# Optimization experiments

Hardware: AMD Instinct MI355X
Metric: run time of the kernel (lower is better)

The kernel has to match this reference:

```python
import jax, jax.numpy as jnp
import numpy as np

N_NODES = 50000
N_EDGES = 800000
IN_CH = 128
HID = 64
PROJ = 32


def _gcn_norm(edge_index, n):
    # add self loops, symmetric normalization D^-1/2 (A+I) D^-1/2
    loop = jnp.arange(n, dtype=edge_index.dtype)
    src = jnp.concatenate([edge_index[0], loop])
    dst = jnp.concatenate([edge_index[1], loop])
    deg = jax.ops.segment_sum(jnp.ones_like(dst, jnp.float32), dst, num_segments=n)
    dinv = deg ** -0.5  # deg >= 1 due to self loops
    norm = dinv[src] * dinv[dst]
    return src, dst, norm


def _propagate(h, src, dst, norm, n):
    # gather -> scale -> scatter-add (message passing along A_hat)
    return jax.ops.segment_sum(h[src] * norm[:, None], dst, num_segments=n)


def _ho_gcn_layer(x, src, dst, norm, Ws, b, n):
    # out = sum_{k=1..max_order} (A_hat^k x) W_k + b
    out = jnp.zeros((n, Ws[0].shape[1]), x.dtype)
    h = x
    for W in Ws:
        h = _propagate(h, src, dst, norm, n)
        out = out + h @ W
    return out + b


def setup_inputs() -> dict:
    key = jax.random.key(0)
    ks = jax.random.split(key, 16)

    def w(k, fan_in, fan_out):
        return (jax.random.normal(k, (fan_in, fan_out), jnp.float32) / np.sqrt(fan_in)).astype(jnp.float32)

    x = jax.random.normal(ks[0], (N_NODES, IN_CH), jnp.float32)
    edge_index = jax.random.randint(ks[1], (2, N_EDGES), 0, N_NODES, dtype=jnp.int64)
    return {
        "x": x,
        "edge_index": edge_index,
        # conv1: max_order=2 -> two weights
        "W1_1": w(ks[2], IN_CH, HID), "W1_2": w(ks[3], IN_CH, HID),
        "b1": jnp.zeros((HID,), jnp.float32),
        # conv2
        "W2_1": w(ks[4], HID, HID // 2), "W2_2": w(ks[5], HID, HID // 2),
        "b2": jnp.zeros((HID // 2,), jnp.float32),
        # projection head
        "Wp1": w(ks[6], HID // 2, PROJ), "bp1": jnp.zeros((PROJ,), jnp.float32),
        "Wp2": w(ks[7], PROJ, PROJ), "bp2": jnp.zeros((PROJ,), jnp.float32),
        # coordinate head
        "Wc1": w(ks[8], HID // 2, HID // 4), "bc1": jnp.zeros((HID // 4,), jnp.float32),
        "Wc2": w(ks[9], HID // 4, 2), "bc2": jnp.zeros((2,), jnp.float32),
    }


def reference(x, edge_index, W1_1, W1_2, b1, W2_1, W2_2, b2,
              Wp1, bp1, Wp2, bp2, Wc1, bc1, Wc2, bc2):
    n = x.shape[0]
    src, dst, norm = _gcn_norm(edge_index, n)
    h1 = jax.nn.relu(_ho_gcn_layer(x, src, dst, norm, (W1_1, W1_2), b1, n))
    # dropout is identity in eval/reference mode
    h2 = jax.nn.relu(_ho_gcn_layer(h1, src, dst, norm, (W2_1, W2_2), b2, n))
    z = jax.nn.relu(h2 @ Wp1 + bp1) @ Wp2 + bp2
    coordinates = jax.nn.relu(h2 @ Wc1 + bc1) @ Wc2 + bc2
    return (coordinates, z)
```

## Files before the change

### kernel.cpp

```cpp
#include <hip/hip_runtime.h>
#include <hip/hip_fp16.h>

#define NN 50000
#define NE 800000
#define S 4
#define BINW 12500
#define NN4 (NN * S)
#define NBLK2 ((NN4 + 255) / 256)
#define NBG ((NN + 63) / 64)
#define NBH4 ((NE / 4 + 255) / 256)
#define COLCAP (NE + 3 * NN4 + 8)

__device__ __forceinline__ float4 ldh4(const __half2* p) {
    float2 raw = *(const float2*)p;
    __half2 a = *(__half2*)&raw.x;
    __half2 b = *(__half2*)&raw.y;
    float2 fa = __half22float2(a);
    float2 fb = __half22float2(b);
    return make_float4(fa.x, fa.y, fb.x, fb.y);
}
__device__ __forceinline__ void sth4(__half2* p, float4 v) {
    __half2 a = __floats2half2_rn(v.x, v.y);
    __half2 b = __floats2half2_rn(v.z, v.w);
    float2 raw;
    raw.x = *(float*)&a; raw.y = *(float*)&b;
    *(float2*)p = raw;
}

__global__ __launch_bounds__(256) void hist_k(const int* __restrict__ src,
                                              const int* __restrict__ dst,
                                              int* __restrict__ cnt,
                                              int* __restrict__ rank) {
    int e = (blockIdx.x * 256 + threadIdx.x) * 4;
    if (e >= NE) return;
    int4 s4 = *(const int4*)(src + e);
    int4 d4 = *(const int4*)(dst + e);
    int4 r;
    r.x = atomicAdd(&cnt[d4.x * S + s4.x / BINW], 1);
    r.y = atomicAdd(&cnt[d4.y * S + s4.y / BINW], 1);
    r.z = atomicAdd(&cnt[d4.z * S + s4.z / BINW], 1);
    r.w = atomicAdd(&cnt[d4.w * S + s4.w / BINW], 1);
    *(int4*)(rank + e) = r;
}

__global__ __launch_bounds__(256) void sum_blocks_k(const int* __restrict__ cnt,
                                                    int* __restrict__ bsum,
                                                    float* __restrict__ dinv,
                                                    unsigned* __restrict__ y2h_s,
                                                    unsigned* __restrict__ uh_s,
                                                    unsigned* __restrict__ z2h_s,
                                                    unsigned* __restrict__ u2h_s) {
    __shared__ int s[256];
    int t = threadIdx.x;
    int i = blockIdx.x * 256 + t;
    if (blockIdx.x == 0) {
        if (t < 32) { y2h_s[t] = 0u; uh_s[t] = 0u; }
        else if (t < 48) { z2h_s[t - 32] = 0u; u2h_s[t - 32] = 0u; }
    }
    int v = 0;
    if (i < NN4) {
        int c = cnt[i];
        v = (c + 3) & ~3;
        if ((i & 3) == 0) {
            int deg = c + cnt[i + 1] + cnt[i + 2] + cnt[i + 3];
            dinv[i >> 2] = rsqrtf((float)(deg + 1));
        }
    }
    s[t] = v;
    __syncthreads();
    for (int off = 128; off > 0; off >>= 1) {
        if (t < off) s[t] += s[t + off];
        __syncthreads();
    }
    if (t == 0) bsum[blockIdx.x] = s[0];
}

__global__ __launch_bounds__(256) void scan_final_k(const int* __restrict__ cnt,
                                                    const int* __restrict__ bsum,
                                                    int* __restrict__ rowsS) {
    __shared__ int sOff[256];
    __shared__ int s[256];
    int t = threadIdx.x;
    int accum = 0;
    for (int idx = t; idx < NBLK2; idx += 256)
        if (idx < blockIdx.x) accum += bsum[idx];
    sOff[t] = accum;
    __syncthreads();
    for (int off = 128; off > 0; off >>= 1) {
        if (t < off) sOff[t] += sOff[t + off];
        __syncthreads();
    }
    int boff = sOff[0];

    int i = blockIdx.x * 256 + t;
    int v = (i < NN4) ? ((cnt[i] + 3) & ~3) : 0;
    s[t] = v;
    __syncthreads();
    for (int off = 1; off < 256; off <<= 1) {
        int x = (t >= off) ? s[t - off] : 0;
        __syncthreads();
        s[t] += x;
        __syncthreads();
    }
    if (i < NN4) rowsS[i] = boff + s[t] - v;
    if (blockIdx.x == NBLK2 - 1 && t == 255) rowsS[NN4] = boff + s[t];
}

__global__ __launch_bounds__(256) void gemm1_scatter_k(const float* __restrict__ A,
                                                       const float* __restrict__ WA,
                                                       const float* __restrict__ WB,
                                                       float* __restrict__ outA,
                                                       __half2* __restrict__ outBh,
                                                       const int* __restrict__ src,
                                                       const int* __restrict__ dst,
                                                       const int* __restrict__ rank,
                                                       const int* __restrict__ rowsS,
                                                       const int* __restrict__ cnt,
                                                       int* __restrict__ col,
                                                       const float* __restrict__ dinv) {
    if (blockIdx.x >= NBG) {
        int idx = (blockIdx.x - NBG) * 256 + threadIdx.x;
        int e = idx * 4;
        if (e < NE) {
            int4 s4 = *(const int4*)(src + e);
            int4 d4 = *(const int4*)(dst + e);
            int4 r4 = *(const int4*)(rank + e);
            col[rowsS[d4.x * S + s4.x / BINW] + r4.x] = s4.x;
            col[rowsS[d4.y * S + s4.y / BINW] + r4.y] = s4.y;
            col[rowsS[d4.z * S + s4.z / BINW] + r4.z] = s4.z;
            col[rowsS[d4.w * S + s4.w / BINW] + r4.w] = s4.w;
        }
        if (idx < NN4) {
            int end = rowsS[idx] + cnt[idx];
            int nxt = rowsS[idx + 1];
            for (int i = end; i < nxt; i++) col[i] = NN;
        }
        return;
    }

    __shared__ float As[64 * 36];
    __shared__ float W1s[32 * 68];
    __shared__ float W2s[32 * 68];
    const int t = threadIdx.x;
    const int tj = t & 15;
    const int tn = t >> 4;
    const int n0 = blockIdx.x * 64;
    float acc[4][8] = {};

    for (int kc = 0; kc < 128; kc += 32) {
        if (kc) __syncthreads();
        {
            int idx = t;
#pragma unroll
            for (int r = 0; r < 2; r++, idx += 256) {
                int nl = idx >> 3, q = idx & 7;
                int node = n0 + nl; node = node < NN ? node : NN - 1;
                float4 a = ((const float4*)A)[(size_t)node * 32 + (kc >> 2) + q];
                *(float4*)&As[nl * 36 + q * 4] = a;
            }
        }
        {
            int idx = t;
#pragma unroll
            for (int r = 0; r < 2; r++, idx += 256) {
                int kl = idx >> 4, j4 = idx & 15;
                *(float4*)&W1s[kl * 68 + j4 * 4] = ((const float4*)WA)[(size_t)(kc + kl) * 16 + j4];
                *(float4*)&W2s[kl * 68 + j4 * 4] = ((const float4*)WB)[(size_t)(kc + kl) * 16 + j4];
            }
        }
        __syncthreads();

        const float* ap = &As[tn * 4 * 36];
        const float* w1p = &W1s[tj * 4];
        const float* w2p = &W2s[tj * 4];
#pragma unroll 2
        for (int k4 = 0; k4 < 8; k4++) {
            float4 a0 = *(const float4*)&ap[0 * 36 + k4 * 4];
            float4 a1 = *(const float4*)&ap[1 * 36 + k4 * 4];
            float4 a2 = *(const float4*)&ap[2 * 36 + k4 * 4];
            float4 a3 = *(const float4*)&ap[3 * 36 + k4 * 4];
#pragma unroll
            for (int kk = 0; kk < 4; kk++) {
                float4 w1 = *(const float4*)&w1p[(k4 * 4 + kk) * 68];
                float4 w2 = *(const float4*)&w2p[(k4 * 4 + kk) * 68];
                float av0 = kk == 0 ? a0.x : kk == 1 ? a0.y : kk == 2 ? a0.z : a0.w;
                float av1 = kk == 0 ? a1.x : kk == 1 ? a1.y : kk == 2 ? a1.z : a1.w;
                float av2 = kk == 0 ? a2.x : kk == 1 ? a2.y : kk == 2 ? a2.z : a2.w;
                float av3 = kk == 0 ? a3.x : kk == 1 ? a3.y : kk == 2 ? a3.z : a3.w;
#define FMA8(m, AV)                                                     \
                acc[m][0] += AV * w1.x; acc[m][1] += AV * w1.y;          \
                acc[m][2] += AV * w1.z; acc[m][3] += AV * w1.w;          \
                acc[m][4] += AV * w2.x; acc[m][5] += AV * w2.y;          \
                acc[m][6] += AV * w2.z; acc[m][7] += AV * w2.w;
                FMA8(0, av0)
                FMA8(1, av1)
                FMA8(2, av2)
                FMA8(3, av3)
#undef FMA8
            }
        }
    }

#pragma unroll
    for (int m = 0; m < 4; m++) {
        int node = n0 + tn * 4 + m;
        if (node < NN) {
            float dnm = dinv[node];
            *(float4*)&outA[(size_t)node * 64 + tj * 4] =
                make_float4(acc[m][0], acc[m][1], acc[m][2], acc[m][3]);
            sth4(outBh + (size_t)node * 32 + tj * 2,
                 make_float4(dnm * acc[m][4], dnm * acc[m][5],
                             dnm * acc[m][6], dnm * acc[m][7]));
        }
    }
}

template<int LOG2C4, bool ADDIN, bool OUTH>
__global__ __launch_bounds__(256) void prop_k(const __half2* __restrict__ hsrc,
                                              const float4* __restrict__ addin4,
                                              const float* __restrict__ bias,
                                              float4* __restrict__ outf,
                                              __half2* __restrict__ outh,
                                              const int* __restrict__ rowsS,
                                              const int* __restrict__ col,
                                              const float* __restrict__ dinv) {
    const int C4 = 1 << LOG2C4;
    const int R2 = 2 * C4;
    unsigned tid = blockIdx.x * blockDim.x + threadIdx.x;
    unsigned node = tid >> LOG2C4;
    if (node >= NN) return;
    unsigned lane = tid & (C4 - 1);
    size_t lane2 = (size_t)lane * 2;
    float dn = dinv[node];
    float4 g = ldh4(hsrc + (size_t)node * R2 + lane2);
    int rs = rowsS[node << 2];
    int re = rowsS[(node << 2) + 4];
    int4 c = *(const int4*)(col + rs);
    for (int i = rs; i < re; i += 4) {
        int4 cc = c;
        c = *(const int4*)(col + i + 4);
        float4 v0 = ldh4(hsrc + (size_t)cc.x * R2 + lane2);
        float4 v1 = ldh4(hsrc + (size_t)cc.y * R2 + lane2);
        float4 v2 = ldh4(hsrc + (size_t)cc.z * R2 + lane2);
        float4 v3 = ldh4(hsrc + (size_t)cc.w * R2 + lane2);
        g.x += v0.x + v1.x + v2.x + v3.x;
        g.y += v0.y + v1.y + v2.y + v3.y;
        g.z += v0.z + v1.z + v2.z + v3.z;
        g.w += v0.w + v1.w + v2.w + v3.w;
    }
    float4 acc;
    if (ADDIN) {
        float4 a = addin4[((size_t)node << LOG2C4) + lane];
        acc.x = dn * (a.x + dn * g.x);
        acc.y = dn * (a.y + dn * g.y);
        acc.z = dn * (a.z + dn * g.z);
        acc.w = dn * (a.w + dn * g.w);
    } else {
        float4 b = ((const float4*)bias)[lane];
        acc.x = fmaxf(b.x + dn * g.x, 0.0f);
        acc.y = fmaxf(b.y + dn * g.y, 0.0f);
        acc.z = fmaxf(b.z + dn * g.z, 0.0f);
        acc.w = fmaxf(b.w + dn * g.w, 0.0f);
    }
    if (OUTH) sth4(outh + (size_t)node * R2 + lane2, acc);
    else      outf[((size_t)node << LOG2C4) + lane] = acc;
}

template<int K, int JW>
__global__ __launch_bounds__(256) void gemm_k(const float* __restrict__ A,
                                              const float* __restrict__ WA,
                                              const float* __restrict__ WB,
                                              float* __restrict__ outA,
                                              __half2* __restrict__ outBh, int n,
                                              const float* __restrict__ dinv) {
    __shared__ float As[64 * 68];
    __shared__ float Ws[64 * 68];
    const int t = threadIdx.x;
    const int tj = t & 15;
    const int tn = t >> 4;
    const int n0 = blockIdx.x * 64;
    float acc[4][4] = {};

    for (int kc = 0; kc < K; kc += 64) {
        if (kc) __syncthreads();
        {
            int idx = t;
#pragma unroll
            for (int r = 0; r < 4; r++, idx += 256) {
                int nl = idx >> 4, q = idx & 15;
                int node = n0 + nl; node = node < n ? node : n - 1;
                float4 a = ((const float4*)A)[(size_t)node * (K / 4) + (kc >> 2) + q];
                *(float4*)&As[nl * 68 + q * 4] = a;
            }
        }
        {
            int idx = t;
#pragma unroll
            for (int r = 0; r < 4; r++, idx += 256) {
                int kl = idx >> 4, j4 = idx & 15;
                const float* W = (j4 < 8) ? WA : WB;
                float4 w = ((const float4*)W)[(size_t)(kc + kl) * 8 + (j4 & 7)];
                *(float4*)&Ws[kl * 68 + j4 * 4] = w;
            }
        }
        __syncthreads();

        const float* ap = &As[tn * 4 * 68];
        const float* wp = &Ws[tj * 4];
#pragma unroll 4
        for (int k4 = 0; k4 < 16; k4++) {
            float4 a0 = *(const float4*)&ap[0 * 68 + k4 * 4];
            float4 a1 = *(const float4*)&ap[1 * 68 + k4 * 4];
            float4 a2 = *(const float4*)&ap[2 * 68 + k4 * 4];
            float4 a3 = *(const float4*)&ap[3 * 68 + k4 * 4];
            float4 w0 = *(const float4*)&wp[(k4 * 4 + 0) * 68];
            float4 w1 = *(const float4*)&wp[(k4 * 4 + 1) * 68];
            float4 w2 = *(const float4*)&wp[(k4 * 4 + 2) * 68];
            float4 w3 = *(const float4*)&wp[(k4 * 4 + 3) * 68];
#define FMA_ROW(m, AV)                                                   \
            acc[m][0] += AV.x * w0.x + AV.y * w1.x + AV.z * w2.x + AV.w * w3.x; \
            acc[m][1] += AV.x * w0.y + AV.y * w1.y + AV.z * w2.y + AV.w * w3.y; \
            acc[m][2] += AV.x * w0.z + AV.y * w1.z + AV.z * w2.z + AV.w * w3.z; \
            acc[m][3] += AV.x * w0.w + AV.y * w1.w + AV.z * w2.w + AV.w * w3.w;
            FMA_ROW(0, a0)
            FMA_ROW(1, a1)
            FMA_ROW(2, a2)
            FMA_ROW(3, a3)
#undef FMA_ROW
        }
    }

    int mat = tj >> 3;
    int jw = tj & 7;
#pragma unroll
    for (int m = 0; m < 4; m++) {
        int node = n0 + tn * 4 + m;
        if (node < n) {
            if (mat) {
                float sc = dinv[node];
                sth4(outBh + (size_t)node * 16 + jw * 2,
                     make_float4(sc * acc[m][0], sc * acc[m][1],
                                 sc * acc[m][2], sc * acc[m][3]));
            } else {
                *(float4*)&outA[(size_t)node * JW + jw * 4] =
                    make_float4(acc[m][0], acc[m][1], acc[m][2], acc[m][3]);
            }
        }
    }
}

__global__ __launch_bounds__(256) void prop_heads_k(const __half2* __restrict__ hsrc,
                                                    const float* __restrict__ b2,
                                                    const int* __restrict__ rowsS,
                                                    const int* __restrict__ col,
                                                    const float* __restrict__ dinv,
                                                    const float* __restrict__ Wp1, const float* __restrict__ bp1,
                                                    const float* __restrict__ Wp2, const float* __restrict__ bp2,
                                                    const float* __restrict__ Wc1, const float* __restrict__ bc1,
                                                    const float* __restrict__ Wc2, const float* __restrict__ bc2,
                                                    float* __restrict__ coord, float* __restrict__ z) {
    __shared__ float sWp1[32 * 32], sWp2[32 * 32], sWc1[32 * 16], sWc2[32];
    __shared__ float sbp1[32], sbp2[32], sbc1[16], sbc2[2];
    __shared__ float sh[32 * 36], st[32 * 36], stc[32 * 18];
    const int t = threadIdx.x;
    for (int i = t; i < 1024; i += 256) { sWp1[i] = Wp1[i]; sWp2[i] = Wp2[i]; }
    for (int i = t; i < 512; i += 256) sWc1[i] = Wc1[i];
    if (t < 32) { sWc2[t] = Wc2[t]; sbp1[t] = bp1[t]; sbp2[t] = bp2[t]; }
    if (t < 16) sbc1[t] = bc1[t];
    if (t < 2) sbc2[t] = bc2[t];

    const int n0 = blockIdx.x * 32;
    const int nl = t >> 3;
    const int jq = t & 7;
    const int node = n0 + nl;

    float4 acc = make_float4(0.f, 0.f, 0.f, 0.f);
    if (node < NN) {
        size_t lane2 = (size_t)jq * 2;
        float dn = dinv[node];
        float4 g = ldh4(hsrc + (size_t)node * 16 + lane2);
        int rs = rowsS[node << 2];
        int re = rowsS[(node << 2) + 4];
        int4 c = *(const int4*)(col + rs);
        for (int i = rs; i < re; i += 4) {
            int4 cc = c;
            c = *(const int4*)(col + i + 4);
            float4 v0 = ldh4(hsrc + (size_t)cc.x * 16 + lane2);
            float4 v1 = ldh4(hsrc + (size_t)cc.y * 16 + lane2);
            float4 v2 = ldh4(hsrc + (size_t)cc.z * 16 + lane2);
            float4 v3 = ldh4(hsrc + (size_t)cc.w * 16 + lane2);
            g.x += v0.x + v1.x + v2.x + v3.x;
            g.y += v0.y + v1.y + v2.y + v3.y;
            g.z += v0.z + v1.z + v2.z + v3.z;
            g.w += v0.w + v1.w + v2.w + v3.w;
        }
        float4 b = ((const float4*)b2)[jq];
        acc.x = fmaxf(b.x + dn * g.x, 0.0f);
        acc.y = fmaxf(b.y + dn * g.y, 0.0f);
        acc.z = fmaxf(b.z + dn * g.z, 0.0f);
        acc.w = fmaxf(b.w + dn * g.w, 0.0f);
    }
    *(float4*)&sh[nl * 36 + jq * 4] = acc;
    __syncthreads();

    float4 a = *(const float4*)&sbp1[jq * 4];
#pragma unroll
    for (int k = 0; k < 32; k++) {
        float hv = sh[nl * 36 + k];
        float4 w = *(const float4*)&sWp1[k * 32 + jq * 4];
        a.x += hv * w.x; a.y += hv * w.y; a.z += hv * w.z; a.w += hv * w.w;
    }
    a.x = fmaxf(a.x, 0.f); a.y = fmaxf(a.y, 0.f);
    a.z = fmaxf(a.z, 0.f); a.w = fmaxf(a.w, 0.f);
    *(float4*)&st[nl * 36 + jq * 4] = a;

    float2 cc2 = *(const float2*)&sbc1[jq * 2];
#pragma unroll
    for (int k = 0; k < 32; k++) {
        float hv = sh[nl * 36 + k];
        float2 w = *(const float2*)&sWc1[k * 16 + jq * 2];
        cc2.x += hv * w.x; cc2.y += hv * w.y;
    }
    cc2.x = fmaxf(cc2.x, 0.f); cc2.y = fmaxf(cc2.y, 0.f);
    *(float2*)&stc[nl * 18 + jq * 2] = cc2;
    __syncthreads();

    float4 zz = *(const float4*)&sbp2[jq * 4];
#pragma unroll
    for (int k = 0; k < 32; k++) {
        float tv = st[nl * 36 + k];
        float4 w = *(const float4*)&sWp2[k * 32 + jq * 4];
        zz.x += tv * w.x; zz.y += tv * w.y; zz.z += tv * w.z; zz.w += tv * w.w;
    }
    if (node < NN) *(float4*)&z[(size_t)node * 32 + jq * 4] = zz;

    if (jq < 2) {
        float s = sbc2[jq];
#pragma unroll
        for (int k = 0; k < 16; k++) s += stc[nl * 18 + k] * sWc2[k * 2 + jq];
        if (node < NN) coord[(size_t)node * 2 + jq] = s;
    }
}

extern "C" void kernel_launch(void* const* d_in, const int* in_sizes, int n_in,
                              void* d_out, int out_size, void* d_ws, size_t ws_size,
                              hipStream_t stream) {
    const float* x    = (const float*)d_in[0];
    const int*   ei   = (const int*)d_in[1];
    const int*   src  = ei;
    const int*   dst  = ei + NE;
    const float* W1_1 = (const float*)d_in[2];
    const float* W1_2 = (const float*)d_in[3];
    const float* b1   = (const float*)d_in[4];
    const float* W2_1 = (const float*)d_in[5];
    const float* W2_2 = (const float*)d_in[6];
    const float* b2   = (const float*)d_in[7];
    const float* Wp1  = (const float*)d_in[8];
    const float* bp1  = (const float*)d_in[9];
    const float* Wp2  = (const float*)d_in[10];
    const float* bp2  = (const float*)d_in[11];
    const float* Wc1  = (const float*)d_in[12];
    const float* bc1  = (const float*)d_in[13];
    const float* Wc2  = (const float*)d_in[14];
    const float* bc2  = (const float*)d_in[15];

    float*   ws    = (float*)d_ws;
    float*   dinv  = ws;
    int*     cnt   = (int*)(ws + 50004);
    int*     rowsS = cnt + NN4;
    int*     bsum  = rowsS + NN4 + 4;
    int*     rank  = bsum + 1024;
    int*     col   = rank + NE;
    float*   y1    = (float*)(col + COLCAP);
    float*   z1    = y1 + (size_t)NN * 64;
    __half2* y2h   = (__half2*)(z1 + (size_t)NN * 32);
    __half2* uh    = y2h + (size_t)(NN + 1) * 32;
    __half2* z2h   = uh + (size_t)(NN + 1) * 32;
    __half2* u2h   = z2h + (size_t)(NN + 1) * 16;
    float*   h1    = y1;

    float* coord = (float*)d_out;
    float* z     = (float*)d_out + 2 * NN;

    hipMemsetAsync(cnt, 0, NN4 * sizeof(int), stream);
    hist_k<<<NBH4, 256, 0, stream>>>(src, dst, cnt, rank);
    sum_blocks_k<<<NBLK2, 256, 0, stream>>>(cnt, bsum, dinv,
                                            (unsigned*)(y2h + (size_t)NN * 32),
                                            (unsigned*)(uh + (size_t)NN * 32),
                                            (unsigned*)(z2h + (size_t)NN * 16),
                                            (unsigned*)(u2h + (size_t)NN * 16));
    scan_final_k<<<NBLK2, 256, 0, stream>>>(cnt, bsum, rowsS);
    gemm1_scatter_k<<<NBG + NBH4, 256, 0, stream>>>(x, W1_1, W1_2, y1, y2h,
                                                    src, dst, rank, rowsS, cnt, col, dinv);

    prop_k<4, true, true><<<(NN * 16 + 255) / 256, 256, 0, stream>>>(
        y2h, (const float4*)y1, nullptr, nullptr, uh, rowsS, col, dinv);
    prop_k<4, false, false><<<(NN * 16 + 255) / 256, 256, 0, stream>>>(
        uh, nullptr, b1, (float4*)h1, nullptr, rowsS, col, dinv);
    gemm_k<64, 32><<<(NN + 63) / 64, 256, 0, stream>>>(h1, W2_1, W2_2, z1, z2h, NN, dinv);
    prop_k<3, true, true><<<(NN * 8 + 255) / 256, 256, 0, stream>>>(
        z2h, (const float4*)z1, nullptr, nullptr, u2h, rowsS, col, dinv);
    prop_heads_k<<<(NN + 31) / 32, 256, 0, stream>>>(
        u2h, b2, rowsS, col, dinv,
        Wp1, bp1, Wp2, bp2, Wc1, bc1, Wc2, bc2, coord, z);
}
```

Before: 257.0 us.

## Split 64-wide half feature tables into two 32-wide planes for propagation

The 64-channel fp16 propagation tables are stored as two separate 32-channel planes, and each first-layer propagation step runs as two launches of the 8-lanes-per-node kernel, one per plane. Each gather then touches a smaller working set (50k×64B per plane), which is meant to raise L2 and last-level cache hit rates for the random neighbour reads. The cost is twice the launches and twice the traversal of the CSR index arrays, and the producing GEMM and the padding-row zeroing change to match the new layout.

```diff
diff --git a/kernel.cpp b/kernel.cpp
--- a/kernel.cpp
+++ b/kernel.cpp
@@ -10,6 +10,7 @@
 #define NBG ((NN + 63) / 64)
 #define NBH4 ((NE / 4 + 255) / 256)
 #define COLCAP (NE + 3 * NN4 + 8)
+#define PLANEH2 ((NN + 1) * 16)
 
 __device__ __forceinline__ float4 ldh4(const __half2* p) {
     float2 raw = *(const float2*)p;
@@ -46,16 +47,18 @@
 __global__ __launch_bounds__(256) void sum_blocks_k(const int* __restrict__ cnt,
                                                     int* __restrict__ bsum,
                                                     float* __restrict__ dinv,
-                                                    unsigned* __restrict__ y2h_s,
-                                                    unsigned* __restrict__ uh_s,
-                                                    unsigned* __restrict__ z2h_s,
-                                                    unsigned* __restrict__ u2h_s) {
+                                                    unsigned* __restrict__ y2s,
+                                                    unsigned* __restrict__ us,
+                                                    unsigned* __restrict__ z2s,
+                                                    unsigned* __restrict__ u2s) {
     __shared__ int s[256];
     int t = threadIdx.x;
     int i = blockIdx.x * 256 + t;
     if (blockIdx.x == 0) {
-        if (t < 32) { y2h_s[t] = 0u; uh_s[t] = 0u; }
-        else if (t < 48) { z2h_s[t - 32] = 0u; u2h_s[t - 32] = 0u; }
+        if (t < 16)      { y2s[t] = 0u;      y2s[PLANEH2 + t] = 0u; }
+        else if (t < 32) { us[t - 16] = 0u;  us[PLANEH2 + t - 16] = 0u; }
+        else if (t < 48) { z2s[t - 32] = 0u; }
+        else if (t < 64) { u2s[t - 48] = 0u; }
     }
     int v = 0;
     if (i < NN4) {
@@ -208,41 +211,39 @@
             float dnm = dinv[node];
             *(float4*)&outA[(size_t)node * 64 + tj * 4] =
                 make_float4(acc[m][0], acc[m][1], acc[m][2], acc[m][3]);
-            sth4(outBh + (size_t)node * 32 + tj * 2,
+            sth4(outBh + (size_t)(tj >> 3) * PLANEH2 + (size_t)node * 16 + (tj & 7) * 2,
                  make_float4(dnm * acc[m][4], dnm * acc[m][5],
                              dnm * acc[m][6], dnm * acc[m][7]));
         }
     }
 }
 
-template<int LOG2C4, bool ADDIN, bool OUTH>
+template<bool ADDIN, bool OUTH>
 __global__ __launch_bounds__(256) void prop_k(const __half2* __restrict__ hsrc,
-                                              const float4* __restrict__ addin4,
+                                              const float4* __restrict__ addin4, int astr4,
                                               const float* __restrict__ bias,
-                                              float4* __restrict__ outf,
+                                              float4* __restrict__ outf, int fstr4,
                                               __half2* __restrict__ outh,
                                               const int* __restrict__ rowsS,
                                               const int* __restrict__ col,
                                               const float* __restrict__ dinv) {
-    const int C4 = 1 << LOG2C4;
-    const int R2 = 2 * C4;
     unsigned tid = blockIdx.x * blockDim.x + threadIdx.x;
-    unsigned node = tid >> LOG2C4;
+    unsigned node = tid >> 3;
     if (node >= NN) return;
-    unsigned lane = tid & (C4 - 1);
+    unsigned lane = tid & 7;
     size_t lane2 = (size_t)lane * 2;
     float dn = dinv[node];
-    float4 g = ldh4(hsrc + (size_t)node * R2 + lane2);
+    float4 g = ldh4(hsrc + (size_t)node * 16 + lane2);
     int rs = rowsS[node << 2];
     int re = rowsS[(node << 2) + 4];
     int4 c = *(const int4*)(col + rs);
     for (int i = rs; i < re; i += 4) {
         int4 cc = c;
         c = *(const int4*)(col + i + 4);
-        float4 v0 = ldh4(hsrc + (size_t)cc.x * R2 + lane2);
-        float4 v1 = ldh4(hsrc + (size_t)cc.y * R2 + lane2);
-        float4 v2 = ldh4(hsrc + (size_t)cc.z * R2 + lane2);
-        float4 v3 = ldh4(hsrc + (size_t)cc.w * R2 + lane2);
+        float4 v0 = ldh4(hsrc + (size_t)cc.x * 16 + lane2);
+        float4 v1 = ldh4(hsrc + (size_t)cc.y * 16 + lane2);
+        float4 v2 = ldh4(hsrc + (size_t)cc.z * 16 + lane2);
+        float4 v3 = ldh4(hsrc + (size_t)cc.w * 16 + lane2);
         g.x += v0.x + v1.x + v2.x + v3.x;
         g.y += v0.y + v1.y + v2.y + v3.y;
         g.z += v0.z + v1.z + v2.z + v3.z;
@@ -250,7 +251,7 @@
     }
     float4 acc;
     if (ADDIN) {
-        float4 a = addin4[((size_t)node << LOG2C4) + lane];
+        float4 a = addin4[(size_t)node * astr4 + lane];
         acc.x = dn * (a.x + dn * g.x);
         acc.y = dn * (a.y + dn * g.y);
         acc.z = dn * (a.z + dn * g.z);
@@ -262,8 +263,8 @@
         acc.z = fmaxf(b.z + dn * g.z, 0.0f);
         acc.w = fmaxf(b.w + dn * g.w, 0.0f);
     }
-    if (OUTH) sth4(outh + (size_t)node * R2 + lane2, acc);
-    else      outf[((size_t)node << LOG2C4) + lane] = acc;
+    if (OUTH) sth4(outh + (size_t)node * 16 + lane2, acc);
+    else      outf[(size_t)node * fstr4 + lane] = acc;
 }
 
 template<int K, int JW>
@@ -474,32 +475,38 @@
     float*   y1    = (float*)(col + COLCAP);
     float*   z1    = y1 + (size_t)NN * 64;
     __half2* y2h   = (__half2*)(z1 + (size_t)NN * 32);
-    __half2* uh    = y2h + (size_t)(NN + 1) * 32;
-    __half2* z2h   = uh + (size_t)(NN + 1) * 32;
-    __half2* u2h   = z2h + (size_t)(NN + 1) * 16;
+    __half2* uh    = y2h + 2 * (size_t)PLANEH2;
+    __half2* z2h   = uh + 2 * (size_t)PLANEH2;
+    __half2* u2h   = z2h + (size_t)PLANEH2;
     float*   h1    = y1;
 
     float* coord = (float*)d_out;
     float* z     = (float*)d_out + 2 * NN;
+
+    const int PG = (NN * 8 + 255) / 256;
 
     hipMemsetAsync(cnt, 0, NN4 * sizeof(int), stream);
     hist_k<<<NBH4, 256, 0, stream>>>(src, dst, cnt, rank);
     sum_blocks_k<<<NBLK2, 256, 0, stream>>>(cnt, bsum, dinv,
-                                            (unsigned*)(y2h + (size_t)NN * 32),
-                                            (unsigned*)(uh + (size_t)NN * 32),
+                                            (unsigned*)(y2h + (size_t)NN * 16),
+                                            (unsigned*)(uh + (size_t)NN * 16),
                                             (unsigned*)(z2h + (size_t)NN * 16),
                                             (unsigned*)(u2h + (size_t)NN * 16));
     scan_final_k<<<NBLK2, 256, 0, stream>>>(cnt, bsum, rowsS);
     gemm1_scatter_k<<<NBG + NBH4, 256, 0, stream>>>(x, W1_1, W1_2, y1, y2h,
                                                     src, dst, rank, rowsS, cnt, col, dinv);
 
-    prop_k<4, true, true><<<(NN * 16 + 255) / 256, 256, 0, stream>>>(
-        y2h, (const float4*)y1, nullptr, nullptr, uh, rowsS, col, dinv);
-    prop_k<4, false, false><<<(NN * 16 + 255) / 256, 256, 0, stream>>>(
-        uh, nullptr, b1, (float4*)h1, nullptr, rowsS, col, dinv);
+    for (int h = 0; h < 2; h++)
+        prop_k<true, true><<<PG, 256, 0, stream>>>(
+            y2h + (size_t)h * PLANEH2, (const float4*)y1 + h * 8, 16,
+            nullptr, nullptr, 0, uh + (size_t)h * PLANEH2, rowsS, col, dinv);
+    for (int h = 0; h < 2; h++)
+        prop_k<false, false><<<PG, 256, 0, stream>>>(
+            uh + (size_t)h * PLANEH2, nullptr, 0,
+            b1 + h * 32, (float4*)h1 + h * 8, 16, nullptr, rowsS, col, dinv);
     gemm_k<64, 32><<<(NN + 63) / 64, 256, 0, stream>>>(h1, W2_1, W2_2, z1, z2h, NN, dinv);
-    prop_k<3, true, true><<<(NN * 8 + 255) / 256, 256, 0, stream>>>(
-        z2h, (const float4*)z1, nullptr, nullptr, u2h, rowsS, col, dinv);
+    prop_k<true, true><<<PG, 256, 0, stream>>>(
+        z2h, (const float4*)z1, 8, nullptr, nullptr, 0, u2h, rowsS, col, dinv);
     prop_heads_k<<<(NN + 31) / 32, 256, 0, stream>>>(
         u2h, b2, rowsS, col, dinv,
         Wp1, bp1, Wp2, bp2, Wc1, bc1, Wc2, bc2, coord, z);
```

Result: slower. 271.1 us (+5.5%).

## Sort nodes by degree to balance work in propagation kernels

Applied to the files above, without the earlier changes.

Builds a degree histogram and a counting-sort permutation of nodes during the CSR construction, then has three propagation kernels process nodes in degree order via the permutation. The goal is to reduce wavefront divergence and load imbalance, since lanes in one wave would then handle rows of similar length. In exchange it adds a single-block scan kernel, atomics and extra index traffic. Output rows are written through the permutation, which scatters the writes.

```diff
diff --git a/kernel.cpp b/kernel.cpp
--- a/kernel.cpp
+++ b/kernel.cpp
@@ -10,6 +10,7 @@
 #define NBG ((NN + 63) / 64)
 #define NBH4 ((NE / 4 + 255) / 256)
 #define COLCAP (NE + 3 * NN4 + 8)
+#define DBINS 512
 
 __device__ __forceinline__ float4 ldh4(const __half2* p) {
     float2 raw = *(const float2*)p;
@@ -46,24 +47,28 @@
 __global__ __launch_bounds__(256) void sum_blocks_k(const int* __restrict__ cnt,
                                                     int* __restrict__ bsum,
                                                     float* __restrict__ dinv,
-                                                    unsigned* __restrict__ y2h_s,
-                                                    unsigned* __restrict__ uh_s,
-                                                    unsigned* __restrict__ z2h_s,
-                                                    unsigned* __restrict__ u2h_s) {
+                                                    int* __restrict__ deg,
+                                                    int* __restrict__ dh,
+                                                    unsigned* __restrict__ y2s,
+                                                    unsigned* __restrict__ us,
+                                                    unsigned* __restrict__ z2s,
+                                                    unsigned* __restrict__ u2s) {
     __shared__ int s[256];
     int t = threadIdx.x;
     int i = blockIdx.x * 256 + t;
     if (blockIdx.x == 0) {
-        if (t < 32) { y2h_s[t] = 0u; uh_s[t] = 0u; }
-        else if (t < 48) { z2h_s[t - 32] = 0u; u2h_s[t - 32] = 0u; }
+        if (t < 32)      { y2s[t] = 0u;      us[t] = 0u; }
+        else if (t < 48) { z2s[t - 32] = 0u; u2s[t - 32] = 0u; }
     }
     int v = 0;
     if (i < NN4) {
         int c = cnt[i];
         v = (c + 3) & ~3;
         if ((i & 3) == 0) {
-            int deg = c + cnt[i + 1] + cnt[i + 2] + cnt[i + 3];
-            dinv[i >> 2] = rsqrtf((float)(deg + 1));
+            int d = c + cnt[i + 1] + cnt[i + 2] + cnt[i + 3];
+            dinv[i >> 2] = rsqrtf((float)(d + 1));
+            deg[i >> 2] = d;
+            atomicAdd(&dh[d < DBINS ? d : DBINS - 1], 1);
         }
     }
     s[t] = v;
@@ -75,12 +80,33 @@
     if (t == 0) bsum[blockIdx.x] = s[0];
 }
 
+__global__ __launch_bounds__(DBINS) void scan_deg_k(int* __restrict__ dh) {
+    __shared__ int s[DBINS];
+    int t = threadIdx.x;
+    int v = dh[t];
+    s[t] = v;
+    __syncthreads();
+    for (int off = 1; off < DBINS; off <<= 1) {
+        int x = (t >= off) ? s[t - off] : 0;
+        __syncthreads();
+        s[t] += x;
+        __syncthreads();
+    }
+    dh[t] = s[t] - v;
+}
+
 __global__ __launch_bounds__(256) void scan_final_k(const int* __restrict__ cnt,
                                                     const int* __restrict__ bsum,
-                                                    int* __restrict__ rowsS) {
+                                                    int* __restrict__ rowsS,
+                                                    const int* __restrict__ deg,
+                                                    int* __restrict__ dh,
+                                                    int* __restrict__ perm) {
     __shared__ int sOff[256];
     __shared__ int s[256];
+    __shared__ int bh[DBINS];
+    __shared__ int bbase[DBINS];
     int t = threadIdx.x;
+    bh[t] = 0; bh[t + 256] = 0;
     int accum = 0;
     for (int idx = t; idx < NBLK2; idx += 256)
         if (idx < blockIdx.x) accum += bsum[idx];
@@ -93,6 +119,20 @@
     int boff = sOff[0];
 
     int i = blockIdx.x * 256 + t;
+    int d = -1, lpos = 0;
+    if (i < NN4 && (i & 3) == 0) {
+        int dd = deg[i >> 2];
+        d = dd < DBINS ? dd : DBINS - 1;
+        lpos = atomicAdd(&bh[d], 1);
+    }
+    __syncthreads();
+    for (int b = t; b < DBINS; b += 256) {
+        int c = bh[b];
+        bbase[b] = c ? atomicAdd(&dh[b], c) : 0;
+    }
+    __syncthreads();
+    if (d >= 0) perm[bbase[d] + lpos] = i >> 2;
+
     int v = (i < NN4) ? ((cnt[i] + 3) & ~3) : 0;
     s[t] = v;
     __syncthreads();
@@ -223,12 +263,14 @@
                                               __half2* __restrict__ outh,
                                               const int* __restrict__ rowsS,
                                               const int* __restrict__ col,
-                                              const float* __restrict__ dinv) {
+                                              const float* __restrict__ dinv,
+                                              const int* __restrict__ perm) {
     const int C4 = 1 << LOG2C4;
     const int R2 = 2 * C4;
     unsigned tid = blockIdx.x * blockDim.x + threadIdx.x;
-    unsigned node = tid >> LOG2C4;
-    if (node >= NN) return;
+    unsigned gi = tid >> LOG2C4;
+    if (gi >= NN) return;
+    unsigned node = (unsigned)perm[gi];
     unsigned lane = tid & (C4 - 1);
     size_t lane2 = (size_t)lane * 2;
     float dn = dinv[node];
@@ -467,7 +509,10 @@
     float*   ws    = (float*)d_ws;
     float*   dinv  = ws;
     int*     cnt   = (int*)(ws + 50004);
-    int*     rowsS = cnt + NN4;
+    int*     dh    = cnt + NN4;
+    int*     deg   = dh + DBINS;
+    int*     perm  = deg + NN;
+    int*     rowsS = perm + NN;
     int*     bsum  = rowsS + NN4 + 4;
     int*     rank  = bsum + 1024;
     int*     col   = rank + NE;
@@ -482,24 +527,25 @@
     float* coord = (float*)d_out;
     float* z     = (float*)d_out + 2 * NN;
 
-    hipMemsetAsync(cnt, 0, NN4 * sizeof(int), stream);
+    hipMemsetAsync(cnt, 0, (NN4 + DBINS) * sizeof(int), stream);
     hist_k<<<NBH4, 256, 0, stream>>>(src, dst, cnt, rank);
-    sum_blocks_k<<<NBLK2, 256, 0, stream>>>(cnt, bsum, dinv,
+    sum_blocks_k<<<NBLK2, 256, 0, stream>>>(cnt, bsum, dinv, deg, dh,
                                             (unsigned*)(y2h + (size_t)NN * 32),
                                             (unsigned*)(uh + (size_t)NN * 32),
                                             (unsigned*)(z2h + (size_t)NN * 16),
                                             (unsigned*)(u2h + (size_t)NN * 16));
-    scan_final_k<<<NBLK2, 256, 0, stream>>>(cnt, bsum, rowsS);
+    scan_deg_k<<<1, DBINS, 0, stream>>>(dh);
+    scan_final_k<<<NBLK2, 256, 0, stream>>>(cnt, bsum, rowsS, deg, dh, perm);
     gemm1_scatter_k<<<NBG + NBH4, 256, 0, stream>>>(x, W1_1, W1_2, y1, y2h,
                                                     src, dst, rank, rowsS, cnt, col, dinv);
 
     prop_k<4, true, true><<<(NN * 16 + 255) / 256, 256, 0, stream>>>(
-        y2h, (const float4*)y1, nullptr, nullptr, uh, rowsS, col, dinv);
+        y2h, (const float4*)y1, nullptr, nullptr, uh, rowsS, col, dinv, perm);
     prop_k<4, false, false><<<(NN * 16 + 255) / 256, 256, 0, stream>>>(
-        uh, nullptr, b1, (float4*)h1, nullptr, rowsS, col, dinv);
+        uh, nullptr, b1, (float4*)h1, nullptr, rowsS, col, dinv, perm);
     gemm_k<64, 32><<<(NN + 63) / 64, 256, 0, stream>>>(h1, W2_1, W2_2, z1, z2h, NN, dinv);
     prop_k<3, true, true><<<(NN * 8 + 255) / 256, 256, 0, stream>>>(
-        z2h, (const float4*)z1, nullptr, nullptr, u2h, rowsS, col, dinv);
+        z2h, (const float4*)z1, nullptr, nullptr, u2h, rowsS, col, dinv, perm);
     prop_heads_k<<<(NN + 31) / 32, 256, 0, stream>>>(
         u2h, b2, rowsS, col, dinv,
         Wp1, bp1, Wp2, bp2, Wc1, bc1, Wc2, bc2, coord, z);
```

New measurement: 425.7 us. +65.7%, slower.
